# Kernel tuning notes

Hardware: AMD Instinct MI355X
Metric: run time of the kernel (lower is better)

Reference implementation:

```python
import jax, jax.numpy as jnp
import numpy as np

N_NODES = 100000
N_EDGES = 1600000
IN_FEA, HIDDEN, RANK = 128, 128, 64


def setup_inputs() -> dict:
    key = jax.random.key(0)
    ks = jax.random.split(key, 6)
    stdv = 1.0 / np.sqrt(HIDDEN)  # reset_parameters uses 1/sqrt(V.size(0)) = 1/sqrt(hidden)
    return {
        "x": jax.random.normal(ks[0], (N_NODES, IN_FEA), dtype=jnp.float32),
        "norm": jax.random.uniform(ks[1], (N_NODES, 1), dtype=jnp.float32),
        "W": jax.random.uniform(ks[2], (IN_FEA, RANK), minval=-stdv, maxval=stdv, dtype=jnp.float32),
        "V": jax.random.uniform(ks[3], (HIDDEN, RANK), minval=-stdv, maxval=stdv, dtype=jnp.float32),
        "src": jax.random.randint(ks[4], (N_EDGES,), 0, N_NODES, dtype=jnp.int32),
        "dst": jax.random.randint(ks[5], (N_EDGES,), 0, N_NODES, dtype=jnp.int32),
    }


def _segment_prod(m, seg, num_segments):
    # product-reduce over ragged mailboxes via sign/log decomposition
    # (numerically equivalent to prod, differentiable: d prod / d m_i = prod / m_i)
    logp = jax.ops.segment_sum(jnp.log(jnp.abs(m)), seg, num_segments=num_segments)
    n_neg = jax.ops.segment_sum((m < 0).astype(m.dtype), seg, num_segments=num_segments)
    sign = 1.0 - 2.0 * jnp.mod(n_neg, 2.0)
    # nodes with no in-edges get logp=0, sign=1 -> product identity 1
    return sign * jnp.exp(logp)


def reference(x, norm, W, V, src, dst):
    n = x.shape[0]
    h = x @ W                      # [N, rank] linear projection
    m = h[src]                     # [E, rank] gather messages along edges
    neigh = _segment_prod(m, dst, n)   # [N, rank] elementwise-product aggregation
    trans_x = norm * neigh         # [N, rank]
    return trans_x @ V.T           # [N, hidden]
```

## Files before the change

kernel.cpp:

```cpp
#include <hip/hip_runtime.h>
#include <hip/hip_bf16.h>

#define N_NODES 100000
#define N_EDGES 1600000
#define IN_FEA 128
#define HIDDEN 128
#define RANK 64

#define NBUCK 391
#define C_BLOCKS 1024
#define EPB 1563
#define S_BLOCKS 256
#define CHUNK_W (EPB * 4)
#define GEMM1_BLOCKS 1563

#define NPW 2
#define AGG_BLOCKS 3125


__device__ __forceinline__ void fma4(float4& a, float s, const float4& b) {
    a.x = fmaf(s, b.x, a.x);
    a.y = fmaf(s, b.y, a.y);
    a.z = fmaf(s, b.z, a.z);
    a.w = fmaf(s, b.w, a.w);
}

__device__ __forceinline__ unsigned short f2bf_rne(float f) {
    unsigned u = __float_as_uint(f);
    u += 0x7fffu + ((u >> 16) & 1u);
    return (unsigned short)(u >> 16);
}

__device__ __forceinline__ float bfu_lo(unsigned u) {
    return __uint_as_float(u << 16);
}
__device__ __forceinline__ float bfu_hi(unsigned u) {
    return __uint_as_float(u & 0xffff0000u);
}


__global__ __launch_bounds__(256) void gemm1_hist_kernel(const float* __restrict__ x,
                                                         const float* __restrict__ W,
                                                         unsigned short* __restrict__ hb,
                                                         const int* __restrict__ dst,
                                                         int* __restrict__ bhist,
                                                         int* __restrict__ blockhist) {
    __shared__ float Wl[IN_FEA * RANK];
    int t = threadIdx.x;

    if (blockIdx.x >= GEMM1_BLOCKS) {
        int* hist = (int*)Wl;
        int b = blockIdx.x - GEMM1_BLOCKS;
        for (int i = t; i < NBUCK; i += 256) hist[i] = 0;
        __syncthreads();
        int b0 = b * EPB;
        int b1 = min(b0 + EPB, N_EDGES);
        for (int e = b0 + t; e < b1; e += 256)
            atomicAdd(&hist[dst[e] >> 8], 1);
        __syncthreads();
        for (int i = t; i < NBUCK; i += 256) {
            int c = hist[i];
            blockhist[b * NBUCK + i] = c;
            if (c) atomicAdd(&bhist[i], c);
        }
        return;
    }

    for (int i = t; i < IN_FEA * RANK; i += 256) Wl[i] = W[i];
    __syncthreads();

    int r0 = (t & 15) * 4;
    int n0 = blockIdx.x * 64 + (t >> 4) * 4;
    const float4* x0 = (const float4*)(x + (long)min(n0 + 0, N_NODES - 1) * IN_FEA);
    const float4* x1 = (const float4*)(x + (long)min(n0 + 1, N_NODES - 1) * IN_FEA);
    const float4* x2 = (const float4*)(x + (long)min(n0 + 2, N_NODES - 1) * IN_FEA);
    const float4* x3 = (const float4*)(x + (long)min(n0 + 3, N_NODES - 1) * IN_FEA);
    float4 a0 = {0.f, 0.f, 0.f, 0.f}, a1 = a0, a2 = a0, a3 = a0;
    for (int k4 = 0; k4 < IN_FEA / 4; ++k4) {
        float4 v0 = x0[k4], v1 = x1[k4], v2 = x2[k4], v3 = x3[k4];
        int kb = k4 * 4;
        float4 w0 = *(const float4*)&Wl[(kb + 0) * RANK + r0];
        float4 w1 = *(const float4*)&Wl[(kb + 1) * RANK + r0];
        float4 w2 = *(const float4*)&Wl[(kb + 2) * RANK + r0];
        float4 w3 = *(const float4*)&Wl[(kb + 3) * RANK + r0];
        fma4(a0, v0.x, w0); fma4(a0, v0.y, w1); fma4(a0, v0.z, w2); fma4(a0, v0.w, w3);
        fma4(a1, v1.x, w0); fma4(a1, v1.y, w1); fma4(a1, v1.z, w2); fma4(a1, v1.w, w3);
        fma4(a2, v2.x, w0); fma4(a2, v2.y, w1); fma4(a2, v2.z, w2); fma4(a2, v2.w, w3);
        fma4(a3, v3.x, w0); fma4(a3, v3.y, w1); fma4(a3, v3.z, w2); fma4(a3, v3.w, w3);
    }
    float4 accs[4] = {a0, a1, a2, a3};
#pragma unroll
    for (int i = 0; i < 4; ++i) {
        if (n0 + i < N_NODES) {
            ushort4 o;
            o.x = f2bf_rne(accs[i].x); o.y = f2bf_rne(accs[i].y);
            o.z = f2bf_rne(accs[i].z); o.w = f2bf_rne(accs[i].w);
            *(ushort4*)(hb + (n0 + i) * RANK + r0) = o;
        }
    }
}


__global__ void bucket_scan_kernel(const int* __restrict__ bhist,
                                   int* __restrict__ bucket_offs,
                                   int* __restrict__ bucket_cursor,
                                   int* __restrict__ offs) {
    __shared__ int sd[512];
    int t = threadIdx.x;
    int v = (t < NBUCK) ? bhist[t] : 0;
    sd[t] = v;
    __syncthreads();
    for (int off = 1; off < 512; off <<= 1) {
        int a = 0;
        if (t >= off) a = sd[t - off];
        __syncthreads();
        sd[t] += a;
        __syncthreads();
    }
    if (t < NBUCK) {
        int excl = sd[t] - v;
        bucket_offs[t] = excl;
        bucket_cursor[t] = excl;
    }
    if (t == 0) {
        bucket_offs[NBUCK] = N_EDGES;
        offs[N_NODES] = N_EDGES;
    }
}

__global__ __launch_bounds__(1024) void binscatter_kernel(const int* __restrict__ src,
                                                          const int* __restrict__ dst,
                                                          const int* __restrict__ blockhist,
                                                          int* __restrict__ bucket_cursor,
                                                          unsigned* __restrict__ pairs) {
    __shared__ int wbase[NBUCK];
    __shared__ int cur[NBUCK];
    int t = threadIdx.x;
    int b = blockIdx.x;
    if (t < NBUCK) {
        int s = 0;
#pragma unroll
        for (int k = 0; k < 4; ++k)
            s += blockhist[(4 * b + k) * NBUCK + t];
        wbase[t] = s ? atomicAdd(&bucket_cursor[t], s) : 0;
        cur[t] = 0;
    }
    __syncthreads();
    int e0 = b * CHUNK_W;
    int e1 = min(e0 + CHUNK_W, N_EDGES);
    for (int e = e0 + t; e < e1; e += 1024) {
        int d = dst[e];
        int s = src[e];
        int bk = d >> 8;
        int lp = atomicAdd(&cur[bk], 1);
        pairs[wbase[bk] + lp] = ((unsigned)s << 8) | (unsigned)(d & 255);
    }
}

__global__ __launch_bounds__(1024) void bucket_build_kernel(const unsigned* __restrict__ pairs,
                                                            const int* __restrict__ bucket_offs,
                                                            int* __restrict__ offs,
                                                            int* __restrict__ eidx) {
    __shared__ int dcnt[256];
    __shared__ int sd[256];
    __shared__ int cur[256];
    int b = blockIdx.x, t = threadIdx.x;
    int base = bucket_offs[b], end = bucket_offs[b + 1];
    if (t < 256) dcnt[t] = 0;
    __syncthreads();
    for (int i = base + t; i < end; i += 1024)
        atomicAdd(&dcnt[pairs[i] & 255u], 1);
    __syncthreads();
    int v = 0;
    if (t < 256) { v = dcnt[t]; sd[t] = v; }
    __syncthreads();
    for (int off = 1; off < 256; off <<= 1) {
        int a = 0;
        if (t >= off && t < 256) a = sd[t - off];
        __syncthreads();
        if (t < 256) sd[t] += a;
        __syncthreads();
    }
    if (t < 256) {
        int excl = sd[t] - v;
        int node = b * 256 + t;
        if (node < N_NODES) offs[node] = base + excl;
        cur[t] = excl;
    }
    __syncthreads();
    for (int i = base + t; i < end; i += 1024) {
        unsigned r = pairs[i];
        int lp = atomicAdd(&cur[r & 255u], 1);
        eidx[base + lp] = (int)(r >> 8);
    }
}


__global__ __launch_bounds__(1024) void agg_gemm_kernel(const unsigned short* __restrict__ hb,
                                                        const float* __restrict__ norm,
                                                        const float* __restrict__ V,
                                                        const int* __restrict__ offs,
                                                        const int* __restrict__ eidx,
                                                        float* __restrict__ out) {
    __shared__ float VL[HIDDEN * 68];
    __shared__ float pls[16][NPW][64];
    int t = threadIdx.x;
    {
        const float4* V4 = (const float4*)V;
#pragma unroll
        for (int k = 0; k < 2; ++k) {
            int i4 = t + 1024 * k;
            float4 v = V4[i4];
            int el = i4 << 2;
            *(float4*)&VL[(el >> 6) * 68 + (el & 63)] = v;
        }
    }
    __syncthreads();

    int wave = t >> 6, lane = t & 63;
    int half = lane >> 5;
    int l32 = lane & 31;
    int nb = (blockIdx.x * 16 + wave) * NPW;
    const unsigned* hb2 = (const unsigned*)hb;

#pragma unroll
    for (int i = 0; i < NPW; ++i) {
        int node = nb + i;
        int beg = offs[node], end = offs[node + 1];

        float plo = 1.0f, phi = 1.0f;
        for (int c = beg; c < end; c += 64) {
            int n = min(64, end - c);
            int sidx = (c + lane < end) ? eidx[c + lane] : 0;
            int j = 0;
            for (; j + 16 <= n; j += 16) {
                int s0 = __shfl(sidx, j + 0  + half);
                int s1 = __shfl(sidx, j + 2  + half);
                int s2 = __shfl(sidx, j + 4  + half);
                int s3 = __shfl(sidx, j + 6  + half);
                int s4 = __shfl(sidx, j + 8  + half);
                int s5 = __shfl(sidx, j + 10 + half);
                int s6 = __shfl(sidx, j + 12 + half);
                int s7 = __shfl(sidx, j + 14 + half);
                unsigned u0 = hb2[(s0 << 5) | l32];
                unsigned u1 = hb2[(s1 << 5) | l32];
                unsigned u2 = hb2[(s2 << 5) | l32];
                unsigned u3 = hb2[(s3 << 5) | l32];
                unsigned u4 = hb2[(s4 << 5) | l32];
                unsigned u5 = hb2[(s5 << 5) | l32];
                unsigned u6 = hb2[(s6 << 5) | l32];
                unsigned u7 = hb2[(s7 << 5) | l32];
                plo *= ((bfu_lo(u0) * bfu_lo(u1)) * (bfu_lo(u2) * bfu_lo(u3))) *
                       ((bfu_lo(u4) * bfu_lo(u5)) * (bfu_lo(u6) * bfu_lo(u7)));
                phi *= ((bfu_hi(u0) * bfu_hi(u1)) * (bfu_hi(u2) * bfu_hi(u3))) *
                       ((bfu_hi(u4) * bfu_hi(u5)) * (bfu_hi(u6) * bfu_hi(u7)));
            }
            for (; j + 8 <= n; j += 8) {
                int s0 = __shfl(sidx, j + 0 + half);
                int s1 = __shfl(sidx, j + 2 + half);
                int s2 = __shfl(sidx, j + 4 + half);
                int s3 = __shfl(sidx, j + 6 + half);
                unsigned u0 = hb2[(s0 << 5) | l32];
                unsigned u1 = hb2[(s1 << 5) | l32];
                unsigned u2 = hb2[(s2 << 5) | l32];
                unsigned u3 = hb2[(s3 << 5) | l32];
                plo *= (bfu_lo(u0) * bfu_lo(u1)) * (bfu_lo(u2) * bfu_lo(u3));
                phi *= (bfu_hi(u0) * bfu_hi(u1)) * (bfu_hi(u2) * bfu_hi(u3));
            }
            for (; j < n; j += 2) {
                int jj = j + half;
                int s = __shfl(sidx, jj);
                unsigned u = hb2[(s << 5) | l32];
                float alo = bfu_lo(u), ahi = bfu_hi(u);
                if (jj >= n) { alo = 1.0f; ahi = 1.0f; }
                plo *= alo;
                phi *= ahi;
            }
        }
        plo *= __shfl_xor(plo, 32);
        phi *= __shfl_xor(phi, 32);

        if (lane < 32) {
            float nrm = norm[node];
            float2 o;
            o.x = plo * nrm;
            o.y = phi * nrm;
            *(float2*)&pls[wave][i][l32 * 2] = o;
        }
    }

    const float4* rA = (const float4*)&VL[lane * 68];
    const float4* rB = (const float4*)&VL[(lane + 64) * 68];
    const float4* p0 = (const float4*)pls[wave][0];
    const float4* p1 = (const float4*)pls[wave][1];
    float aA0 = 0.f, aB0 = 0.f, aA1 = 0.f, aB1 = 0.f;
#pragma unroll
    for (int q = 0; q < 16; ++q) {
        float4 va = rA[q];
        float4 vb = rB[q];
        float4 pp;
        pp = p0[q];
        aA0 = fmaf(pp.x, va.x, fmaf(pp.y, va.y, fmaf(pp.z, va.z, fmaf(pp.w, va.w, aA0))));
        aB0 = fmaf(pp.x, vb.x, fmaf(pp.y, vb.y, fmaf(pp.z, vb.z, fmaf(pp.w, vb.w, aB0))));
        pp = p1[q];
        aA1 = fmaf(pp.x, va.x, fmaf(pp.y, va.y, fmaf(pp.z, va.z, fmaf(pp.w, va.w, aA1))));
        aB1 = fmaf(pp.x, vb.x, fmaf(pp.y, vb.y, fmaf(pp.z, vb.z, fmaf(pp.w, vb.w, aB1))));
    }
    out[(nb + 0) * HIDDEN + lane]      = aA0;
    out[(nb + 0) * HIDDEN + 64 + lane] = aB0;
    out[(nb + 1) * HIDDEN + lane]      = aA1;
    out[(nb + 1) * HIDDEN + 64 + lane] = aB1;
}


extern "C" void kernel_launch(void* const* d_in, const int* in_sizes, int n_in,
                              void* d_out, int out_size, void* d_ws, size_t ws_size,
                              hipStream_t stream) {
    const float* x    = (const float*)d_in[0];
    const float* norm = (const float*)d_in[1];
    const float* W    = (const float*)d_in[2];
    const float* V    = (const float*)d_in[3];
    const int*   src  = (const int*)d_in[4];
    const int*   dst  = (const int*)d_in[5];
    float* out = (float*)d_out;

    unsigned short* hb = (unsigned short*)d_ws;
    int*   offs        = (int*)(hb + (long)N_NODES * RANK);
    int*   eidx        = offs + N_NODES + 1;
    int*   bhist       = eidx + N_EDGES;
    int*   bucket_offs = bhist + NBUCK;
    int*   bucket_cur  = bucket_offs + NBUCK + 1;

    unsigned* pairs    = (unsigned*)d_out;
    int*     blockhist = (int*)d_out + 2097152;

    hipMemsetAsync(bhist, 0, NBUCK * sizeof(int), stream);
    gemm1_hist_kernel<<<GEMM1_BLOCKS + C_BLOCKS, 256, 0, stream>>>(x, W, hb, dst, bhist, blockhist);
    bucket_scan_kernel<<<1, 512, 0, stream>>>(bhist, bucket_offs, bucket_cur, offs);
    binscatter_kernel<<<S_BLOCKS, 1024, 0, stream>>>(src, dst, blockhist, bucket_cur, pairs);
    bucket_build_kernel<<<NBUCK, 1024, 0, stream>>>(pairs, bucket_offs, offs, eidx);
    agg_gemm_kernel<<<AGG_BLOCKS, 1024, 0, stream>>>(hb, norm, V, offs, eidx, out);
}
```

Measured before the change: 246.0 us.

## Fold bucket scan into histogram blocks, vectorize binscatter, use readlane in agg GEMM

New measurement: 360.9 us. 1.47x slower.

```diff
diff --git a/kernel.cpp b/kernel.cpp
--- a/kernel.cpp
+++ b/kernel.cpp
@@ -38,14 +38,23 @@
     return __uint_as_float(u & 0xffff0000u);
 }
 
+__device__ __forceinline__ float rdlane(float v, int l) {
+    return __uint_as_float(__builtin_amdgcn_readlane(__float_as_uint(v), l));
+}
+
 
 __global__ __launch_bounds__(256) void gemm1_hist_kernel(const float* __restrict__ x,
                                                          const float* __restrict__ W,
                                                          unsigned short* __restrict__ hb,
                                                          const int* __restrict__ dst,
                                                          int* __restrict__ bhist,
-                                                         int* __restrict__ blockhist) {
+                                                         int* __restrict__ blockhist,
+                                                         int* __restrict__ done,
+                                                         int* __restrict__ bucket_offs,
+                                                         int* __restrict__ bucket_cursor,
+                                                         int* __restrict__ offs) {
     __shared__ float Wl[IN_FEA * RANK];
+    __shared__ int lastf;
     int t = threadIdx.x;
 
     if (blockIdx.x >= GEMM1_BLOCKS) {
@@ -62,6 +71,31 @@
             int c = hist[i];
             blockhist[b * NBUCK + i] = c;
             if (c) atomicAdd(&bhist[i], c);
+        }
+        __threadfence();
+        if (t == 0) lastf = (atomicAdd(done, 1) == C_BLOCKS - 1) ? 1 : 0;
+        __syncthreads();
+        if (!lastf) return;
+        __threadfence();
+        int* sa = hist + 512;
+        int* sb = sa + 512;
+        for (int i = t; i < NBUCK; i += 256) sa[i] = bhist[i];
+        __syncthreads();
+        int* pin = sa; int* pout = sb;
+        for (int off = 1; off < NBUCK; off <<= 1) {
+            for (int i = t; i < NBUCK; i += 256)
+                pout[i] = (i >= off) ? pin[i] + pin[i - off] : pin[i];
+            __syncthreads();
+            int* tmp = pin; pin = pout; pout = tmp;
+        }
+        for (int i = t; i < NBUCK; i += 256) {
+            int excl = pin[i] - bhist[i];
+            bucket_offs[i] = excl;
+            bucket_cursor[i] = excl;
+        }
+        if (t == 0) {
+            bucket_offs[NBUCK] = N_EDGES;
+            offs[N_NODES] = N_EDGES;
         }
         return;
     }
@@ -101,33 +135,6 @@
 }
 
 
-__global__ void bucket_scan_kernel(const int* __restrict__ bhist,
-                                   int* __restrict__ bucket_offs,
-                                   int* __restrict__ bucket_cursor,
-                                   int* __restrict__ offs) {
-    __shared__ int sd[512];
-    int t = threadIdx.x;
-    int v = (t < NBUCK) ? bhist[t] : 0;
-    sd[t] = v;
-    __syncthreads();
-    for (int off = 1; off < 512; off <<= 1) {
-        int a = 0;
-        if (t >= off) a = sd[t - off];
-        __syncthreads();
-        sd[t] += a;
-        __syncthreads();
-    }
-    if (t < NBUCK) {
-        int excl = sd[t] - v;
-        bucket_offs[t] = excl;
-        bucket_cursor[t] = excl;
-    }
-    if (t == 0) {
-        bucket_offs[NBUCK] = N_EDGES;
-        offs[N_NODES] = N_EDGES;
-    }
-}
-
 __global__ __launch_bounds__(1024) void binscatter_kernel(const int* __restrict__ src,
                                                           const int* __restrict__ dst,
                                                           const int* __restrict__ blockhist,
@@ -148,12 +155,15 @@
     __syncthreads();
     int e0 = b * CHUNK_W;
     int e1 = min(e0 + CHUNK_W, N_EDGES);
-    for (int e = e0 + t; e < e1; e += 1024) {
-        int d = dst[e];
-        int s = src[e];
-        int bk = d >> 8;
-        int lp = atomicAdd(&cur[bk], 1);
-        pairs[wbase[bk] + lp] = ((unsigned)s << 8) | (unsigned)(d & 255);
+    for (int e = e0 + t * 2; e < e1; e += 2048) {
+        int2 d2 = *(const int2*)&dst[e];
+        int2 s2 = *(const int2*)&src[e];
+        int bk0 = d2.x >> 8;
+        int lp0 = atomicAdd(&cur[bk0], 1);
+        pairs[wbase[bk0] + lp0] = ((unsigned)s2.x << 8) | (unsigned)(d2.x & 255);
+        int bk1 = d2.y >> 8;
+        int lp1 = atomicAdd(&cur[bk1], 1);
+        pairs[wbase[bk1] + lp1] = ((unsigned)s2.y << 8) | (unsigned)(d2.y & 255);
     }
 }
 
@@ -203,7 +213,6 @@
                                                         const int* __restrict__ eidx,
                                                         float* __restrict__ out) {
     __shared__ float VL[HIDDEN * 68];
-    __shared__ float pls[16][NPW][64];
     int t = threadIdx.x;
     {
         const float4* V4 = (const float4*)V;
@@ -223,6 +232,7 @@
     int nb = (blockIdx.x * 16 + wave) * NPW;
     const unsigned* hb2 = (const unsigned*)hb;
 
+    float plo0, phi0, plo1, phi1;
 #pragma unroll
     for (int i = 0; i < NPW; ++i) {
         int node = nb + i;
@@ -280,31 +290,31 @@
         plo *= __shfl_xor(plo, 32);
         phi *= __shfl_xor(phi, 32);
 
-        if (lane < 32) {
-            float nrm = norm[node];
-            float2 o;
-            o.x = plo * nrm;
-            o.y = phi * nrm;
-            *(float2*)&pls[wave][i][l32 * 2] = o;
-        }
+        float nrm = norm[node];
+        plo *= nrm;
+        phi *= nrm;
+        if (i == 0) { plo0 = plo; phi0 = phi; } else { plo1 = plo; phi1 = phi; }
     }
 
     const float4* rA = (const float4*)&VL[lane * 68];
     const float4* rB = (const float4*)&VL[(lane + 64) * 68];
-    const float4* p0 = (const float4*)pls[wave][0];
-    const float4* p1 = (const float4*)pls[wave][1];
     float aA0 = 0.f, aB0 = 0.f, aA1 = 0.f, aB1 = 0.f;
 #pragma unroll
     for (int q = 0; q < 16; ++q) {
         float4 va = rA[q];
         float4 vb = rB[q];
-        float4 pp;
-        pp = p0[q];
-        aA0 = fmaf(pp.x, va.x, fmaf(pp.y, va.y, fmaf(pp.z, va.z, fmaf(pp.w, va.w, aA0))));
-        aB0 = fmaf(pp.x, vb.x, fmaf(pp.y, vb.y, fmaf(pp.z, vb.z, fmaf(pp.w, vb.w, aB0))));
-        pp = p1[q];
-        aA1 = fmaf(pp.x, va.x, fmaf(pp.y, va.y, fmaf(pp.z, va.z, fmaf(pp.w, va.w, aA1))));
-        aB1 = fmaf(pp.x, vb.x, fmaf(pp.y, vb.y, fmaf(pp.z, vb.z, fmaf(pp.w, vb.w, aB1))));
+        float px = rdlane(plo0, 2 * q);
+        float py = rdlane(phi0, 2 * q);
+        float pz = rdlane(plo0, 2 * q + 1);
+        float pw = rdlane(phi0, 2 * q + 1);
+        aA0 = fmaf(px, va.x, fmaf(py, va.y, fmaf(pz, va.z, fmaf(pw, va.w, aA0))));
+        aB0 = fmaf(px, vb.x, fmaf(py, vb.y, fmaf(pz, vb.z, fmaf(pw, vb.w, aB0))));
+        px = rdlane(plo1, 2 * q);
+        py = rdlane(phi1, 2 * q);
+        pz = rdlane(plo1, 2 * q + 1);
+        pw = rdlane(phi1, 2 * q + 1);
+        aA1 = fmaf(px, va.x, fmaf(py, va.y, fmaf(pz, va.z, fmaf(pw, va.w, aA1))));
+        aB1 = fmaf(px, vb.x, fmaf(py, vb.y, fmaf(pz, vb.z, fmaf(pw, vb.w, aB1))));
     }
     out[(nb + 0) * HIDDEN + lane]      = aA0;
     out[(nb + 0) * HIDDEN + 64 + lane] = aB0;
@@ -328,15 +338,16 @@
     int*   offs        = (int*)(hb + (long)N_NODES * RANK);
     int*   eidx        = offs + N_NODES + 1;
     int*   bhist       = eidx + N_EDGES;
-    int*   bucket_offs = bhist + NBUCK;
+    int*   done        = bhist + NBUCK;
+    int*   bucket_offs = done + 1;
     int*   bucket_cur  = bucket_offs + NBUCK + 1;
 
     unsigned* pairs    = (unsigned*)d_out;
     int*     blockhist = (int*)d_out + 2097152;
 
-    hipMemsetAsync(bhist, 0, NBUCK * sizeof(int), stream);
-    gemm1_hist_kernel<<<GEMM1_BLOCKS + C_BLOCKS, 256, 0, stream>>>(x, W, hb, dst, bhist, blockhist);
-    bucket_scan_kernel<<<1, 512, 0, stream>>>(bhist, bucket_offs, bucket_cur, offs);
+    hipMemsetAsync(bhist, 0, (NBUCK + 1) * sizeof(int), stream);
+    gemm1_hist_kernel<<<GEMM1_BLOCKS + C_BLOCKS, 256, 0, stream>>>(
+        x, W, hb, dst, bhist, blockhist, done, bucket_offs, bucket_cur, offs);
     binscatter_kernel<<<S_BLOCKS, 1024, 0, stream>>>(src, dst, blockhist, bucket_cur, pairs);
     bucket_build_kernel<<<NBUCK, 1024, 0, stream>>>(pairs, bucket_offs, offs, eidx);
     agg_gemm_kernel<<<AGG_BLOCKS, 1024, 0, stream>>>(hb, norm, V, offs, eidx, out);
```
